# Performance work log

Measured on AMD Instinct MI355X. Metric: run time of the kernel, lower is better.

## Reference

```python
import jax, jax.numpy as jnp
import numpy as np


def _to_class(x):
    # x: (B, T, 1) -> class in {0,1,2,3}: (<0)->0, [0,1)->1, [1,2)->2, (>=2)->3
    return (jnp.clip(jnp.floor(x[..., 0]), -1.0, 2.0) + 1.0).astype(jnp.int32)


def setup_inputs() -> dict:
    key = jax.random.key(0)
    k1, k2, k3 = jax.random.split(key, 3)
    B, T = 524288, 48
    pred = jax.random.normal(k1, (B, T, 1), dtype=jnp.float32) * 1.5
    true = jax.random.normal(k2, (B, T, 1), dtype=jnp.float32) * 1.5
    score_matrix = jax.random.uniform(k3, (4, 4), dtype=jnp.float32) * 3.0
    return {"pred": pred, "true": true, "score_matrix": score_matrix}


def reference(pred, true, score_matrix):
    # normalize exp(-S) over all 16 entries
    e = jnp.exp(-score_matrix)
    sm = e / jnp.sum(e)  # (4, 4)
    pred_cls = _to_class(pred)  # (B, T) int32
    true_cls = _to_class(true)  # (B, T) int32
    gmgs_weight = sm[true_cls, pred_cls]  # (B, T) gather into 4x4 table
    sq = jnp.square(pred - true)[..., 0]  # (B, T)
    loss = jnp.sum(sq * gmgs_weight) / pred.shape[0]
    return loss
```

## Files before the change

kernel.cpp:

```cpp
#include <hip/hip_runtime.h>

#define BLOCK 256
#define GRID 2048

__device__ __forceinline__ int gmgs_cls(float x) {
    float f = fminf(fmaxf(floorf(x), -1.0f), 2.0f);
    return (int)f + 1;
}

__global__ __launch_bounds__(BLOCK) void gmgs_partial_kernel(
    const float* __restrict__ pred,
    const float* __restrict__ tru,
    const float* __restrict__ score,
    float* __restrict__ partials,
    int n4, int rem)
{
    __shared__ float sm_e[16];
    __shared__ float sred[BLOCK / 64];
    __shared__ float s_inv;

    const int tid = threadIdx.x;

    if (tid < 16) sm_e[tid] = expf(-score[tid]);
    __syncthreads();
    if (tid == 0) {
        float s = 0.0f;
        #pragma unroll
        for (int i = 0; i < 16; ++i) s += sm_e[i];
        s_inv = 1.0f / s;
    }
    __syncthreads();
    const float inv_norm = s_inv;

    const float4* __restrict__ pred4 = (const float4*)pred;
    const float4* __restrict__ tru4  = (const float4*)tru;

    float acc = 0.0f;
    const int stride = gridDim.x * blockDim.x;
    for (int i = blockIdx.x * blockDim.x + tid; i < n4; i += stride) {
        float4 p = pred4[i];
        float4 t = tru4[i];
        #pragma unroll
        for (int k = 0; k < 4; ++k) {
            float pv = (&p.x)[k];
            float tv = (&t.x)[k];
            int pc = gmgs_cls(pv);
            int tc = gmgs_cls(tv);
            float d = pv - tv;
            acc += d * d * sm_e[tc * 4 + pc];
        }
    }

    if (blockIdx.x == 0 && tid < rem) {
        int i = n4 * 4 + tid;
        float pv = pred[i];
        float tv = tru[i];
        int pc = gmgs_cls(pv);
        int tc = gmgs_cls(tv);
        float d = pv - tv;
        acc += d * d * sm_e[tc * 4 + pc];
    }

    #pragma unroll
    for (int off = 32; off > 0; off >>= 1)
        acc += __shfl_down(acc, off, 64);

    if ((tid & 63) == 0) sred[tid >> 6] = acc;
    __syncthreads();
    if (tid == 0) {
        float s = 0.0f;
        #pragma unroll
        for (int w = 0; w < BLOCK / 64; ++w) s += sred[w];
        partials[blockIdx.x] = s * inv_norm;
    }
}

__global__ __launch_bounds__(1024) void gmgs_final_kernel(
    const float* __restrict__ partials,
    float* __restrict__ out,
    int nblocks, float invB)
{
    __shared__ float sred[1024 / 64];
    const int tid = threadIdx.x;

    float acc = 0.0f;
    for (int i = tid; i < nblocks; i += blockDim.x) acc += partials[i];

    #pragma unroll
    for (int off = 32; off > 0; off >>= 1)
        acc += __shfl_down(acc, off, 64);

    if ((tid & 63) == 0) sred[tid >> 6] = acc;
    __syncthreads();
    if (tid == 0) {
        float s = 0.0f;
        #pragma unroll
        for (int w = 0; w < 1024 / 64; ++w) s += sred[w];
        out[0] = s * invB;
    }
}

extern "C" void kernel_launch(void* const* d_in, const int* in_sizes, int n_in,
                              void* d_out, int out_size, void* d_ws, size_t ws_size,
                              hipStream_t stream) {
    const float* pred  = (const float*)d_in[0];
    const float* tru   = (const float*)d_in[1];
    const float* score = (const float*)d_in[2];
    float* out = (float*)d_out;
    float* partials = (float*)d_ws;

    long long n = (long long)in_sizes[0];
    int n4  = (int)(n >> 2);
    int rem = (int)(n & 3);
    long long B = n / 48;
    float invB = 1.0f / (float)B;

    gmgs_partial_kernel<<<GRID, BLOCK, 0, stream>>>(pred, tru, score, partials, n4, rem);
    gmgs_final_kernel<<<1, 1024, 0, stream>>>(partials, out, GRID, invB);
}
```

Before: 215.3 us.

## Fuse final reduction via atomicAdd and unroll grid-stride loads by four

Replaces the second reduction kernel with a per-block atomicAdd into the output, which is zeroed beforehand with a memset. The grid-stride loop is unrolled four ways with independent accumulators so more loads are in flight per thread. The exp-sum normalization moves into the block epilogue. Float atomics make the summation order nondeterministic, and the memset adds a separate operation on the stream.

```diff
diff --git a/kernel.cpp b/kernel.cpp
--- a/kernel.cpp
+++ b/kernel.cpp
@@ -3,64 +3,64 @@
 #define BLOCK 256
 #define GRID 2048
 
-__device__ __forceinline__ int gmgs_cls(float x) {
-    float f = fminf(fmaxf(floorf(x), -1.0f), 2.0f);
-    return (int)f + 1;
+__device__ __forceinline__ float gmgs_term(float pv, float tv, const float* __restrict__ sm_e) {
+    float pf = fminf(fmaxf(floorf(pv), -1.0f), 2.0f);
+    float tf = fminf(fmaxf(floorf(tv), -1.0f), 2.0f);
+    int pc = (int)pf + 1;
+    int tc = (int)tf + 1;
+    float d = pv - tv;
+    return d * d * sm_e[tc * 4 + pc];
 }
 
-__global__ __launch_bounds__(BLOCK) void gmgs_partial_kernel(
+__device__ __forceinline__ float gmgs_quad(float4 p, float4 t, const float* __restrict__ sm_e) {
+    return (gmgs_term(p.x, t.x, sm_e) + gmgs_term(p.y, t.y, sm_e))
+         + (gmgs_term(p.z, t.z, sm_e) + gmgs_term(p.w, t.w, sm_e));
+}
+
+__global__ __launch_bounds__(BLOCK) void gmgs_loss_kernel(
     const float* __restrict__ pred,
     const float* __restrict__ tru,
     const float* __restrict__ score,
-    float* __restrict__ partials,
-    int n4, int rem)
+    float* __restrict__ out,
+    int n4, int rem, float invB)
 {
     __shared__ float sm_e[16];
     __shared__ float sred[BLOCK / 64];
-    __shared__ float s_inv;
 
     const int tid = threadIdx.x;
-
     if (tid < 16) sm_e[tid] = expf(-score[tid]);
     __syncthreads();
-    if (tid == 0) {
-        float s = 0.0f;
-        #pragma unroll
-        for (int i = 0; i < 16; ++i) s += sm_e[i];
-        s_inv = 1.0f / s;
-    }
-    __syncthreads();
-    const float inv_norm = s_inv;
 
     const float4* __restrict__ pred4 = (const float4*)pred;
     const float4* __restrict__ tru4  = (const float4*)tru;
 
-    float acc = 0.0f;
-    const int stride = gridDim.x * blockDim.x;
-    for (int i = blockIdx.x * blockDim.x + tid; i < n4; i += stride) {
-        float4 p = pred4[i];
-        float4 t = tru4[i];
-        #pragma unroll
-        for (int k = 0; k < 4; ++k) {
-            float pv = (&p.x)[k];
-            float tv = (&t.x)[k];
-            int pc = gmgs_cls(pv);
-            int tc = gmgs_cls(tv);
-            float d = pv - tv;
-            acc += d * d * sm_e[tc * 4 + pc];
-        }
+    const int stride = GRID * BLOCK;
+    int i = (int)blockIdx.x * BLOCK + tid;
+    float acc0 = 0.0f, acc1 = 0.0f, acc2 = 0.0f, acc3 = 0.0f;
+
+    for (; i + 3 * stride < n4; i += 4 * stride) {
+        float4 p0 = pred4[i];
+        float4 p1 = pred4[i + stride];
+        float4 p2 = pred4[i + 2 * stride];
+        float4 p3 = pred4[i + 3 * stride];
+        float4 t0 = tru4[i];
+        float4 t1 = tru4[i + stride];
+        float4 t2 = tru4[i + 2 * stride];
+        float4 t3 = tru4[i + 3 * stride];
+        acc0 += gmgs_quad(p0, t0, sm_e);
+        acc1 += gmgs_quad(p1, t1, sm_e);
+        acc2 += gmgs_quad(p2, t2, sm_e);
+        acc3 += gmgs_quad(p3, t3, sm_e);
+    }
+    for (; i < n4; i += stride)
+        acc0 += gmgs_quad(pred4[i], tru4[i], sm_e);
+
+    if (blockIdx.x == 0 && tid < rem) {
+        int j = n4 * 4 + tid;
+        acc0 += gmgs_term(pred[j], tru[j], sm_e);
     }
 
-    if (blockIdx.x == 0 && tid < rem) {
-        int i = n4 * 4 + tid;
-        float pv = pred[i];
-        float tv = tru[i];
-        int pc = gmgs_cls(pv);
-        int tc = gmgs_cls(tv);
-        float d = pv - tv;
-        acc += d * d * sm_e[tc * 4 + pc];
-    }
-
+    float acc = (acc0 + acc1) + (acc2 + acc3);
     #pragma unroll
     for (int off = 32; off > 0; off >>= 1)
         acc += __shfl_down(acc, off, 64);
@@ -71,32 +71,10 @@
         float s = 0.0f;
         #pragma unroll
         for (int w = 0; w < BLOCK / 64; ++w) s += sred[w];
-        partials[blockIdx.x] = s * inv_norm;
-    }
-}
-
-__global__ __launch_bounds__(1024) void gmgs_final_kernel(
-    const float* __restrict__ partials,
-    float* __restrict__ out,
-    int nblocks, float invB)
-{
-    __shared__ float sred[1024 / 64];
-    const int tid = threadIdx.x;
-
-    float acc = 0.0f;
-    for (int i = tid; i < nblocks; i += blockDim.x) acc += partials[i];
-
-    #pragma unroll
-    for (int off = 32; off > 0; off >>= 1)
-        acc += __shfl_down(acc, off, 64);
-
-    if ((tid & 63) == 0) sred[tid >> 6] = acc;
-    __syncthreads();
-    if (tid == 0) {
-        float s = 0.0f;
+        float e = 0.0f;
         #pragma unroll
-        for (int w = 0; w < 1024 / 64; ++w) s += sred[w];
-        out[0] = s * invB;
+        for (int k = 0; k < 16; ++k) e += sm_e[k];
+        atomicAdd(out, s * invB / e);
     }
 }
 
@@ -107,7 +85,6 @@
     const float* tru   = (const float*)d_in[1];
     const float* score = (const float*)d_in[2];
     float* out = (float*)d_out;
-    float* partials = (float*)d_ws;
 
     long long n = (long long)in_sizes[0];
     int n4  = (int)(n >> 2);
@@ -115,6 +92,6 @@
     long long B = n / 48;
     float invB = 1.0f / (float)B;
 
-    gmgs_partial_kernel<<<GRID, BLOCK, 0, stream>>>(pred, tru, score, partials, n4, rem);
-    gmgs_final_kernel<<<1, 1024, 0, stream>>>(partials, out, GRID, invB);
+    hipMemsetAsync(d_out, 0, sizeof(float), stream);
+    gmgs_loss_kernel<<<GRID, BLOCK, 0, stream>>>(pred, tru, score, out, n4, rem, invB);
 }
```

After: 218.7 us. About the same (+1.6%).

## Use one-float4-per-thread grid and move normalization into final reduction

Applied to the files above, without the earlier changes.

Replaces the fixed 2048-block grid-stride loop with a grid of one float4 pair per thread, so about 24.5K blocks of 256 threads are launched. The per-block normalization sum and its extra barrier move into the single-block final kernel, which now recomputes the exp sum once. The intent is more memory-level parallelism and less per-block overhead. In exchange there are many more blocks, each repeating the shared-table exp setup, and the final kernel reduces about 24K partials serially per thread.

```diff
diff --git a/kernel.cpp b/kernel.cpp
--- a/kernel.cpp
+++ b/kernel.cpp
@@ -1,14 +1,18 @@
 #include <hip/hip_runtime.h>
 
-#define BLOCK 256
-#define GRID 2048
+#define S1_BLOCK 256
+#define S2_BLOCK 1024
 
-__device__ __forceinline__ int gmgs_cls(float x) {
-    float f = fminf(fmaxf(floorf(x), -1.0f), 2.0f);
-    return (int)f + 1;
+__device__ __forceinline__ float gmgs_term(float pv, float tv, const float* __restrict__ sm_e) {
+    int pc = (int)fminf(fmaxf(floorf(pv), -1.0f), 2.0f) + 1;
+    int tc = (int)fminf(fmaxf(floorf(tv), -1.0f), 2.0f) + 1;
+    float d = pv - tv;
+    return d * d * sm_e[(tc << 2) | pc];
 }
 
-__global__ __launch_bounds__(BLOCK) void gmgs_partial_kernel(
+__global__ __launch_bounds__(S1_BLOCK) void gmgs_stage1(
+    const float4* __restrict__ pred4,
+    const float4* __restrict__ tru4,
     const float* __restrict__ pred,
     const float* __restrict__ tru,
     const float* __restrict__ score,
@@ -16,49 +20,23 @@
     int n4, int rem)
 {
     __shared__ float sm_e[16];
-    __shared__ float sred[BLOCK / 64];
-    __shared__ float s_inv;
+    __shared__ float sred[S1_BLOCK / 64];
 
     const int tid = threadIdx.x;
-
     if (tid < 16) sm_e[tid] = expf(-score[tid]);
     __syncthreads();
-    if (tid == 0) {
-        float s = 0.0f;
-        #pragma unroll
-        for (int i = 0; i < 16; ++i) s += sm_e[i];
-        s_inv = 1.0f / s;
-    }
-    __syncthreads();
-    const float inv_norm = s_inv;
 
-    const float4* __restrict__ pred4 = (const float4*)pred;
-    const float4* __restrict__ tru4  = (const float4*)tru;
-
+    const int i = (int)blockIdx.x * S1_BLOCK + tid;
     float acc = 0.0f;
-    const int stride = gridDim.x * blockDim.x;
-    for (int i = blockIdx.x * blockDim.x + tid; i < n4; i += stride) {
+    if (i < n4) {
         float4 p = pred4[i];
         float4 t = tru4[i];
-        #pragma unroll
-        for (int k = 0; k < 4; ++k) {
-            float pv = (&p.x)[k];
-            float tv = (&t.x)[k];
-            int pc = gmgs_cls(pv);
-            int tc = gmgs_cls(tv);
-            float d = pv - tv;
-            acc += d * d * sm_e[tc * 4 + pc];
-        }
+        acc = (gmgs_term(p.x, t.x, sm_e) + gmgs_term(p.y, t.y, sm_e))
+            + (gmgs_term(p.z, t.z, sm_e) + gmgs_term(p.w, t.w, sm_e));
     }
-
     if (blockIdx.x == 0 && tid < rem) {
-        int i = n4 * 4 + tid;
-        float pv = pred[i];
-        float tv = tru[i];
-        int pc = gmgs_cls(pv);
-        int tc = gmgs_cls(tv);
-        float d = pv - tv;
-        acc += d * d * sm_e[tc * 4 + pc];
+        int j = n4 * 4 + tid;
+        acc += gmgs_term(pred[j], tru[j], sm_e);
     }
 
     #pragma unroll
@@ -70,21 +48,22 @@
     if (tid == 0) {
         float s = 0.0f;
         #pragma unroll
-        for (int w = 0; w < BLOCK / 64; ++w) s += sred[w];
-        partials[blockIdx.x] = s * inv_norm;
+        for (int w = 0; w < S1_BLOCK / 64; ++w) s += sred[w];
+        partials[blockIdx.x] = s;
     }
 }
 
-__global__ __launch_bounds__(1024) void gmgs_final_kernel(
+__global__ __launch_bounds__(S2_BLOCK) void gmgs_stage2(
     const float* __restrict__ partials,
+    const float* __restrict__ score,
     float* __restrict__ out,
-    int nblocks, float invB)
+    int nblk, float invB)
 {
-    __shared__ float sred[1024 / 64];
+    __shared__ float sred[S2_BLOCK / 64];
     const int tid = threadIdx.x;
 
     float acc = 0.0f;
-    for (int i = tid; i < nblocks; i += blockDim.x) acc += partials[i];
+    for (int i = tid; i < nblk; i += S2_BLOCK) acc += partials[i];
 
     #pragma unroll
     for (int off = 32; off > 0; off >>= 1)
@@ -95,8 +74,11 @@
     if (tid == 0) {
         float s = 0.0f;
         #pragma unroll
-        for (int w = 0; w < 1024 / 64; ++w) s += sred[w];
-        out[0] = s * invB;
+        for (int w = 0; w < S2_BLOCK / 64; ++w) s += sred[w];
+        float z = 0.0f;
+        #pragma unroll
+        for (int k = 0; k < 16; ++k) z += expf(-score[k]);
+        out[0] = s * invB / z;
     }
 }
 
@@ -115,6 +97,9 @@
     long long B = n / 48;
     float invB = 1.0f / (float)B;
 
-    gmgs_partial_kernel<<<GRID, BLOCK, 0, stream>>>(pred, tru, score, partials, n4, rem);
-    gmgs_final_kernel<<<1, 1024, 0, stream>>>(partials, out, GRID, invB);
+    int nblk = (n4 + S1_BLOCK - 1) / S1_BLOCK;
+
+    gmgs_stage1<<<nblk, S1_BLOCK, 0, stream>>>(
+        (const float4*)pred, (const float4*)tru, pred, tru, score, partials, n4, rem);
+    gmgs_stage2<<<1, S2_BLOCK, 0, stream>>>(partials, score, out, nblk, invB);
 }
```

Measured after the change: 216.4 us. About the same (+0.5%).
